# Kernel tuning notes

Measured on AMD Instinct MI355X. Metric: run time of the kernel, lower is better.

Reference implementation:

```python
import jax, jax.numpy as jnp
import numpy as np

# ---- static module configuration (matches init_kwargs) ----
INPUT_SIZE = 123256
N_SYS = 4            # number of subsystems N
SKIP_RES = 4
PATCH = 30
SKIP = 10
FACTOR_FAKE = 3.0
NOISE = 0.5
CUTOFF = 0.5
BATCH = 256

N_RES = int(-0.5 + np.sqrt(0.25 + 2 * INPUT_SIZE)) + SKIP_RES          # 500
NB_PER_RES = int(np.ceil(PATCH / SKIP))                                 # 3
BALANCE = N_RES % SKIP // 2                                             # 0
_starts = (np.arange(N_RES) + BALANCE) // SKIP
BS_PER_RES = _starts[:, None] + np.arange(NB_PER_RES)[None, :]          # (n_res, nb)
NUM_WEIGHTS = int(BS_PER_RES[-1, -1] + 1)                               # 52
RES1, RES2 = np.triu_indices(N_RES, k=SKIP_RES)                         # (P,), (P,) P = INPUT_SIZE
assert RES1.shape[0] == INPUT_SIZE


def setup_inputs() -> dict:
    key = jax.random.key(0)
    k1, k2, k3 = jax.random.split(key, 3)
    x = jax.random.normal(k1, (BATCH, INPUT_SIZE), dtype=jnp.float32)
    mean = jax.random.normal(k2, (1, INPUT_SIZE), dtype=jnp.float32)
    std = jnp.ones((1, INPUT_SIZE), dtype=jnp.float32)
    weights = jax.random.normal(k3, (N_SYS, NUM_WEIGHTS), dtype=jnp.float32)
    return {"x": x, "mean": mean, "std": std, "weights": weights}


def _get_softmax(weights):
    # weights: (N, W). torch: softmax per subsystem over W, scale by W,
    # gather nb_per_res bins per residue and take their product.
    p = jax.nn.softmax(weights, axis=1) * NUM_WEIGHTS              # (N, W)
    w_res = jnp.prod(p[:, BS_PER_RES], axis=-1).T                  # (n_res, N)
    fake = jnp.full((N_RES, 1), FACTOR_FAKE, dtype=w_res.dtype)
    w_all = jnp.concatenate([w_res, fake], axis=1)                 # (n_res, N+1)
    w_all = jax.nn.relu(w_all - CUTOFF)
    w_all = w_all / jnp.sum(w_all, axis=1, keepdims=True)
    return w_all[:, :N_SYS]                                        # (n_res, N)


def reference(x, mean, std, weights):
    xn = (x - mean) / std                                          # (B, P)
    w = _get_softmax(weights)                                      # (n_res, N)
    prod = N_SYS + 1
    # gather per-pair residue weights; outer-product mask
    alpha = (w[RES1] * prod) * (w[RES2] * prod)                    # (P, N)
    masked = xn[:, :, None] * alpha[None, :, :]                    # (B, P, N)
    if NOISE > 0.0:
        max_a = jax.lax.stop_gradient(jnp.max(alpha, axis=0, keepdims=True))  # (1, N)
        rnd = jax.random.normal(jax.random.key(42), masked.shape, masked.dtype) * NOISE
        masked = masked + (1.0 - alpha / max_a)[None, :, :] * rnd
    # torch returns torch.split(masked, 1, dim=2) -> N views; we return the
    # stacked tensor (identical values, contiguous layout).
    return masked
```

## Files before the change

### kernel.cpp

```cpp
#include <hip/hip_runtime.h>
#include <stdint.h>

#define NRES    500
#define SKIPRES 4
#define PCOUNT  123256
#define NSYS    4
#define NW      52
#define BATCH   256

__global__ void prep_kernel(const float* __restrict__ weights,
                            float* __restrict__ ws) {
    __shared__ float pbuf[NSYS][NW];
    __shared__ float vsh[NRES][NSYS];
    const int tid = threadIdx.x;

    if (tid < NSYS) {
        const int s = tid;
        float m = -1e30f;
        for (int k = 0; k < NW; ++k) m = fmaxf(m, weights[s * NW + k]);
        float sum = 0.f;
        for (int k = 0; k < NW; ++k) {
            float e = expf(weights[s * NW + k] - m);
            pbuf[s][k] = e;
            sum += e;
        }
        float scale = (float)NW / sum;
        for (int k = 0; k < NW; ++k) pbuf[s][k] *= scale;
    }
    __syncthreads();

    for (int r = tid; r < NRES; r += blockDim.x) {
        const int st = r / 10;
        float a[NSYS];
        float denom = 2.5f;
        for (int s = 0; s < NSYS; ++s) {
            float wr = pbuf[s][st] * pbuf[s][st + 1] * pbuf[s][st + 2];
            float t = wr - 0.5f;
            t = t > 0.f ? t : 0.f;
            a[s] = t;
            denom += t;
        }
        const float inv = 1.0f / denom;
        for (int s = 0; s < NSYS; ++s) vsh[r][s] = 5.0f * a[s] * inv;
    }
    __syncthreads();

    if (tid < NSYS) {
        const int s = tid;
        float m = 0.f, best = 0.f;
        for (int i = NRES - 1 - SKIPRES; i >= 0; --i) {
            m = fmaxf(m, vsh[i + SKIPRES][s]);
            best = fmaxf(best, vsh[i][s] * m);
        }
        ws[s] = 1.0f / best;
    }
    float4* vout = (float4*)(ws + 4);
    for (int r = tid; r < NRES; r += blockDim.x) {
        vout[r] = make_float4(vsh[r][0], vsh[r][1], vsh[r][2], vsh[r][3]);
    }
}

__device__ __forceinline__ uint32_t rotl32(uint32_t x, int d) {
    return (x << d) | (x >> (32 - d));
}

__device__ __forceinline__ uint32_t tf_bits(uint32_t c1) {
    const uint32_t ks0 = 0u;
    const uint32_t ks1 = 42u;
    const uint32_t ks2 = 0x1BD11BDAu ^ 0u ^ 42u;
    uint32_t x0 = 0u + ks0;
    uint32_t x1 = c1 + ks1;
#define TF_RND(d) { x0 += x1; x1 = rotl32(x1, (d)); x1 ^= x0; }
    TF_RND(13) TF_RND(15) TF_RND(26) TF_RND(6)
    x0 += ks1; x1 += ks2 + 1u;
    TF_RND(17) TF_RND(29) TF_RND(16) TF_RND(24)
    x0 += ks2; x1 += ks0 + 2u;
    TF_RND(13) TF_RND(15) TF_RND(26) TF_RND(6)
    x0 += ks0; x1 += ks1 + 3u;
    TF_RND(17) TF_RND(29) TF_RND(16) TF_RND(24)
    x0 += ks1; x1 += ks2 + 4u;
    TF_RND(13) TF_RND(15) TF_RND(26) TF_RND(6)
    x0 += ks2; x1 += ks0 + 5u;
#undef TF_RND
    return x0 ^ x1;
}

__device__ __forceinline__ float u_from_bits(uint32_t b) {
    const float lo = -0.99999994f;
    float f = __uint_as_float((b >> 9) | 0x3F800000u) - 1.0f;
    float u = fmaf(f, 2.0f, lo);
    return fmaxf(lo, u);
}

__device__ __forceinline__ float erfinv_xla(float x) {
    float w = -__logf(1.0f - x * x);
    float p;
    if (w < 5.0f) {
        w = w - 2.5f;
        p =              2.81022636e-08f;
        p = fmaf(p, w,   3.43273939e-07f);
        p = fmaf(p, w,  -3.5233877e-06f);
        p = fmaf(p, w,  -4.39150654e-06f);
        p = fmaf(p, w,   0.00021858087f);
        p = fmaf(p, w,  -0.00125372503f);
        p = fmaf(p, w,  -0.00417768164f);
        p = fmaf(p, w,   0.246640727f);
        p = fmaf(p, w,   1.50140941f);
    } else {
        w = __fsqrt_rn(w) - 3.0f;
        p =             -0.000200214257f;
        p = fmaf(p, w,   0.000100950558f);
        p = fmaf(p, w,   0.00134934322f);
        p = fmaf(p, w,  -0.00367342844f);
        p = fmaf(p, w,   0.00573950773f);
        p = fmaf(p, w,  -0.0076224613f);
        p = fmaf(p, w,   0.00943887047f);
        p = fmaf(p, w,   1.00167406f);
        p = fmaf(p, w,   2.83297682f);
    }
    return p * x;
}

__device__ __forceinline__ float normal_from_bits(uint32_t b) {
    return 1.41421356237f * erfinv_xla(u_from_bits(b));
}

__global__ __launch_bounds__(256)
void mask_kernel(const float* __restrict__ x,
                 const float* __restrict__ mean,
                 const float* __restrict__ stdv,
                 const float* __restrict__ ws,
                 float* __restrict__ out) {
    const int p = blockIdx.x * 256 + threadIdx.x;
    if (p >= PCOUNT) return;
    const int b = blockIdx.y;

    float disc = 246512.25f - 2.0f * (float)p;
    int i = (int)(496.5f - __fsqrt_rn(disc));
    if (i < 0) i = 0;
    if (i > NRES - SKIPRES - 1) i = NRES - SKIPRES - 1;
#define CUM(ii) (((ii) * (993 - (ii))) >> 1)
    while (i > 0 && p < CUM(i)) --i;
    while (i < NRES - SKIPRES - 1 && p >= CUM(i + 1)) ++i;
    const int j = p - CUM(i) + i + SKIPRES;
#undef CUM

    const float4* v4 = (const float4*)(ws + 4);
    const float4 vi = v4[i];
    const float4 vj = v4[j];
    const float im0 = ws[0], im1 = ws[1], im2 = ws[2], im3 = ws[3];

    const float a0 = vi.x * vj.x;
    const float a1 = vi.y * vj.y;
    const float a2 = vi.z * vj.z;
    const float a3 = vi.w * vj.w;
    const float c0 = fmaf(-a0, im0, 1.0f) * 0.5f;
    const float c1 = fmaf(-a1, im1, 1.0f) * 0.5f;
    const float c2 = fmaf(-a2, im2, 1.0f) * 0.5f;
    const float c3 = fmaf(-a3, im3, 1.0f) * 0.5f;

    const float mu = mean[p];
    const float sd = stdv[p];
    const uint32_t bp = (uint32_t)b * PCOUNT + (uint32_t)p;
    const float xn = (x[bp] - mu) / sd;

    const uint32_t base = bp * 4u;
    const float r0 = normal_from_bits(tf_bits(base + 0u));
    const float r1 = normal_from_bits(tf_bits(base + 1u));
    const float r2 = normal_from_bits(tf_bits(base + 2u));
    const float r3 = normal_from_bits(tf_bits(base + 3u));

    float4 o;
    o.x = fmaf(xn, a0, c0 * r0);
    o.y = fmaf(xn, a1, c1 * r1);
    o.z = fmaf(xn, a2, c2 * r2);
    o.w = fmaf(xn, a3, c3 * r3);

    ((float4*)out)[bp] = o;
}

extern "C" void kernel_launch(void* const* d_in, const int* in_sizes, int n_in,
                              void* d_out, int out_size, void* d_ws, size_t ws_size,
                              hipStream_t stream) {
    const float* x       = (const float*)d_in[0];
    const float* mean    = (const float*)d_in[1];
    const float* stdv    = (const float*)d_in[2];
    const float* weights = (const float*)d_in[3];
    float* ws  = (float*)d_ws;
    float* out = (float*)d_out;

    hipLaunchKernelGGL(prep_kernel, dim3(1), dim3(256), 0, stream, weights, ws);

    dim3 grid((PCOUNT + 255) / 256, BATCH);
    hipLaunchKernelGGL(mask_kernel, grid, dim3(256), 0, stream,
                       x, mean, stdv, ws, out);
}
```

Measured before the change: 824.0 us.

## Precompute per-pair alpha/noise-scale tables and process four batch rows per thread

Measured after the change: 729.5 us. -11.5%, faster.

```diff
diff --git a/kernel.cpp b/kernel.cpp
--- a/kernel.cpp
+++ b/kernel.cpp
@@ -7,6 +7,8 @@
 #define NSYS    4
 #define NW      52
 #define BATCH   256
+#define NB      4
+
 
 __global__ void prep_kernel(const float* __restrict__ weights,
                             float* __restrict__ ws) {
@@ -58,6 +60,58 @@
     for (int r = tid; r < NRES; r += blockDim.x) {
         vout[r] = make_float4(vsh[r][0], vsh[r][1], vsh[r][2], vsh[r][3]);
     }
+}
+
+__device__ __forceinline__ void decode_pair(int p, int& oi, int& oj) {
+    float disc = 246512.25f - 2.0f * (float)p;
+    int i = (int)(496.5f - __fsqrt_rn(disc));
+    if (i < 0) i = 0;
+    if (i > NRES - SKIPRES - 1) i = NRES - SKIPRES - 1;
+#define CUM(ii) (((ii) * (993 - (ii))) >> 1)
+    while (i > 0 && p < CUM(i)) --i;
+    while (i < NRES - SKIPRES - 1 && p >= CUM(i + 1)) ++i;
+    oj = p - CUM(i) + i + SKIPRES;
+#undef CUM
+    oi = i;
+}
+
+__global__ __launch_bounds__(256)
+void table_kernel(const float* __restrict__ mean,
+                  const float* __restrict__ stdv,
+                  const float* __restrict__ ws,
+                  float4* __restrict__ atab,
+                  float4* __restrict__ ctab,
+                  float2* __restrict__ ntab) {
+    const int p = blockIdx.x * 256 + threadIdx.x;
+    if (p >= PCOUNT) return;
+
+    int i, j;
+    decode_pair(p, i, j);
+
+    const float4* v4 = (const float4*)(ws + 4);
+    const float4 vi = v4[i];
+    const float4 vj = v4[j];
+    const float im0 = ws[0], im1 = ws[1], im2 = ws[2], im3 = ws[3];
+
+    float4 a;
+    a.x = vi.x * vj.x;
+    a.y = vi.y * vj.y;
+    a.z = vi.z * vj.z;
+    a.w = vi.w * vj.w;
+
+    const float K = 0.5f * 1.41421356237f;
+    float4 c;
+    c.x = fmaf(-a.x, im0, 1.0f) * K;
+    c.y = fmaf(-a.y, im1, 1.0f) * K;
+    c.z = fmaf(-a.z, im2, 1.0f) * K;
+    c.w = fmaf(-a.w, im3, 1.0f) * K;
+
+    atab[p] = a;
+    ctab[p] = c;
+
+    const float sd = stdv[p];
+    const float ooSd = 1.0f / sd;
+    ntab[p] = make_float2(-mean[p] * ooSd, ooSd);
 }
 
 __device__ __forceinline__ uint32_t rotl32(uint32_t x, int d) {
@@ -126,6 +180,42 @@
 }
 
 __global__ __launch_bounds__(256)
+void mask_kernel_tab(const float* __restrict__ x,
+                     const float4* __restrict__ atab,
+                     const float4* __restrict__ ctab,
+                     const float2* __restrict__ ntab,
+                     float* __restrict__ out) {
+    const int p = blockIdx.x * 256 + threadIdx.x;
+    if (p >= PCOUNT) return;
+
+    const float4 a = atab[p];
+    const float4 c = ctab[p];
+    const float2 nr = ntab[p];
+
+    uint32_t bp = (uint32_t)(blockIdx.y * NB) * (uint32_t)PCOUNT + (uint32_t)p;
+    float4* o4 = (float4*)out;
+
+#pragma unroll
+    for (int k = 0; k < NB; ++k) {
+        const float xn = fmaf(x[bp], nr.y, nr.x);
+        const uint32_t base = bp * 4u;
+        const float r0 = erfinv_xla(u_from_bits(tf_bits(base + 0u)));
+        const float r1 = erfinv_xla(u_from_bits(tf_bits(base + 1u)));
+        const float r2 = erfinv_xla(u_from_bits(tf_bits(base + 2u)));
+        const float r3 = erfinv_xla(u_from_bits(tf_bits(base + 3u)));
+
+        float4 o;
+        o.x = fmaf(xn, a.x, c.x * r0);
+        o.y = fmaf(xn, a.y, c.y * r1);
+        o.z = fmaf(xn, a.z, c.z * r2);
+        o.w = fmaf(xn, a.w, c.w * r3);
+        o4[bp] = o;
+
+        bp += (uint32_t)PCOUNT;
+    }
+}
+
+__global__ __launch_bounds__(256)
 void mask_kernel(const float* __restrict__ x,
                  const float* __restrict__ mean,
                  const float* __restrict__ stdv,
@@ -135,15 +225,8 @@
     if (p >= PCOUNT) return;
     const int b = blockIdx.y;
 
-    float disc = 246512.25f - 2.0f * (float)p;
-    int i = (int)(496.5f - __fsqrt_rn(disc));
-    if (i < 0) i = 0;
-    if (i > NRES - SKIPRES - 1) i = NRES - SKIPRES - 1;
-#define CUM(ii) (((ii) * (993 - (ii))) >> 1)
-    while (i > 0 && p < CUM(i)) --i;
-    while (i < NRES - SKIPRES - 1 && p >= CUM(i + 1)) ++i;
-    const int j = p - CUM(i) + i + SKIPRES;
-#undef CUM
+    int i, j;
+    decode_pair(p, i, j);
 
     const float4* v4 = (const float4*)(ws + 4);
     const float4 vi = v4[i];
@@ -191,7 +274,27 @@
 
     hipLaunchKernelGGL(prep_kernel, dim3(1), dim3(256), 0, stream, weights, ws);
 
-    dim3 grid((PCOUNT + 255) / 256, BATCH);
-    hipLaunchKernelGGL(mask_kernel, grid, dim3(256), 0, stream,
-                       x, mean, stdv, ws, out);
-}
+    const size_t ATAB_OFF = 8192;
+    const size_t CTAB_OFF = ATAB_OFF + (size_t)PCOUNT * 16;
+    const size_t NTAB_OFF = CTAB_OFF + (size_t)PCOUNT * 16;
+    const size_t NEED     = NTAB_OFF + (size_t)PCOUNT * 8;
+
+    const dim3 gx((PCOUNT + 255) / 256);
+
+    if (ws_size >= NEED) {
+        float4* atab = (float4*)((char*)d_ws + ATAB_OFF);
+        float4* ctab = (float4*)((char*)d_ws + CTAB_OFF);
+        float2* ntab = (float2*)((char*)d_ws + NTAB_OFF);
+
+        hipLaunchKernelGGL(table_kernel, gx, dim3(256), 0, stream,
+                           mean, stdv, ws, atab, ctab, ntab);
+
+        dim3 grid(gx.x, BATCH / NB);
+        hipLaunchKernelGGL(mask_kernel_tab, grid, dim3(256), 0, stream,
+                           x, atab, ctab, ntab, out);
+    } else {
+        dim3 grid(gx.x, BATCH);
+        hipLaunchKernelGGL(mask_kernel, grid, dim3(256), 0, stream,
+                           x, mean, stdv, ws, out);
+    }
+}
```
